# Performance work log

Measured on AMD Instinct MI355X. Metric: run time of the kernel, lower is better.

## Reference

```python
import jax, jax.numpy as jnp
import numpy as np

# dims
B, T, F, R, H = 2048, 50, 64, 6, 64      # batch, time, features, num_rims, hidden per rim
KS, VS = 64, 128                          # input attention key/query size, value size
NC, QC, VC = 4, 32, 16                    # comm heads, comm key/query size, comm value (NC*VC == H)
S = 16                                    # static features
K_ACT = 4                                 # active rims (top-k routing)


def setup_inputs() -> dict:
    key = jax.random.key(0)
    ks = jax.random.split(key, 24)
    f32 = jnp.float32
    rn = lambda k, shape, scale: jax.random.normal(k, shape, f32) * scale
    inp = {}
    inp['x'] = jax.random.normal(ks[0], (B, T, F), f32)
    inp['statics'] = jax.random.normal(ks[1], (B, S), f32)
    inp['mask'] = (jax.random.uniform(ks[2], (B, T, F)) > 0.3).astype(f32)
    inp['delta'] = jax.random.uniform(ks[3], (B, T, F), f32) * 5.0
    inp['x_last_observed'] = jax.random.normal(ks[4], (B, T, F), f32)
    inp['x_mean'] = jax.random.normal(ks[5], (B, F), f32)
    # GRU-D style per-feature input decay params
    inp['w_dg'] = rn(ks[6], (F,), 0.1)
    inp['b_dg'] = jnp.zeros((F,), f32)
    # input attention (shared K/V over the 2-slot [input, null] axis; per-rim group query)
    inp['Wk'] = rn(ks[7], (F, KS), 1.0 / np.sqrt(F))
    inp['Wv'] = rn(ks[8], (F, VS), 1.0 / np.sqrt(F))
    inp['Wq'] = rn(ks[9], (R, H, KS), 1.0 / np.sqrt(H))
    # per-rim (group) GRU cell
    inp['W_ih'] = rn(ks[10], (R, VS, 3 * H), 1.0 / np.sqrt(VS))
    inp['W_hh'] = rn(ks[11], (R, H, 3 * H), 1.0 / np.sqrt(H))
    inp['b_ih'] = jnp.zeros((R, 3 * H), f32)
    inp['b_hh'] = jnp.zeros((R, 3 * H), f32)
    # communication attention (per-rim group projections)
    inp['Wq_c'] = rn(ks[12], (R, H, NC * QC), 1.0 / np.sqrt(H))
    inp['Wk_c'] = rn(ks[13], (R, H, NC * QC), 1.0 / np.sqrt(H))
    inp['Wv_c'] = rn(ks[14], (R, H, NC * VC), 1.0 / np.sqrt(H))
    # MLP head
    inp['W1'] = rn(ks[15], (R * H + S, 10), 1.0 / np.sqrt(R * H + S))
    inp['b1'] = jnp.zeros((10,), f32)
    inp['W2'] = rn(ks[16], (10, 2), 1.0 / np.sqrt(10))
    inp['b2'] = jnp.zeros((2,), f32)
    return inp


def reference(x, statics, mask, delta, x_last_observed, x_mean,
              w_dg, b_dg, Wk, Wv, Wq, W_ih, W_hh, b_ih, b_hh,
              Wq_c, Wk_c, Wv_c, W1, b1, W2, b2):
    Bn = x.shape[0]
    inv_sk = 1.0 / np.sqrt(KS).astype(np.float32)
    inv_sq = 1.0 / np.sqrt(QC).astype(np.float32)

    def step(h, inp_t):
        xt, mt, dt, xlt = inp_t  # each [B,F]
        # GRU-D input decay / imputation
        gamma = jnp.exp(-jax.nn.relu(dt * w_dg + b_dg))
        xh = mt * xt + (1.0 - mt) * (gamma * xlt + (1.0 - gamma) * x_mean)
        # input attention over [real, null] slots
        x_in = jnp.stack([xh, jnp.zeros_like(xh)], axis=1)          # [B,2,F]
        Km = x_in @ Wk                                               # [B,2,KS]
        Vm = x_in @ Wv                                               # [B,2,VS]
        Q = jnp.einsum('brh,rhk->brk', h, Wq)                        # [B,R,KS]
        probs = jax.nn.softmax(jnp.einsum('brk,bnk->brn', Q, Km) * inv_sk, axis=-1)  # [B,R,2]
        inputs = jnp.einsum('brn,bnv->brv', probs, Vm)               # [B,R,VS]
        # top-k active rims = least attention to the null slot
        act_idx = jax.lax.top_k(-probs[:, :, 1], K_ACT)[1]           # [B,K_ACT]
        rim_mask = jnp.sum(jax.nn.one_hot(act_idx, R, dtype=h.dtype), axis=1)  # [B,R]
        # per-rim GRU update (blocked GEMMs)
        gi = jnp.einsum('brv,rvg->brg', inputs, W_ih) + b_ih         # [B,R,3H]
        gh = jnp.einsum('brh,rhg->brg', h, W_hh) + b_hh              # [B,R,3H]
        i_r, i_z, i_n = jnp.split(gi, 3, axis=-1)
        h_r, h_z, h_n = jnp.split(gh, 3, axis=-1)
        r = jax.nn.sigmoid(i_r + h_r)
        z = jax.nn.sigmoid(i_z + h_z)
        n = jnp.tanh(i_n + r * h_n)
        h_new = (1.0 - z) * n + z * h                                # [B,R,H]
        # communication attention among rims
        q = jnp.einsum('brh,rhk->brk', h_new, Wq_c).reshape(Bn, R, NC, QC).transpose(0, 2, 1, 3)
        k = jnp.einsum('brh,rhk->brk', h_new, Wk_c).reshape(Bn, R, NC, QC).transpose(0, 2, 1, 3)
        v = jnp.einsum('brh,rhk->brk', h_new, Wv_c).reshape(Bn, R, NC, VC).transpose(0, 2, 1, 3)
        cprobs = jax.nn.softmax(jnp.einsum('bcrk,bcsk->bcrs', q, k) * inv_sq, axis=-1)  # [B,NC,R,R]
        comm = jnp.einsum('bcrs,bcsv->bcrv', cprobs, v).transpose(0, 2, 1, 3).reshape(Bn, R, NC * VC)
        # only active rims are updated (and receive comm); inactive keep old state
        m = rim_mask[..., None]
        h_out = m * (h_new + comm) + (1.0 - m) * h
        return h_out, None

    h0 = jnp.zeros((Bn, R, H), x.dtype)
    seq = (x.transpose(1, 0, 2), mask.transpose(1, 0, 2),
           delta.transpose(1, 0, 2), x_last_observed.transpose(1, 0, 2))
    hT, _ = jax.lax.scan(step, h0, seq)
    full = jnp.concatenate([hT.reshape(Bn, R * H), statics], axis=1)
    predictions = jax.nn.relu(full @ W1 + b1) @ W2 + b2              # [B,2]
    return predictions
```

## Files before the change

### kernel.cpp

```cpp
#include <hip/hip_runtime.h>
#include <math.h>

#define T_STEPS 50
#define BB 8

__device__ __forceinline__ void fma4(float4& a, const float4 v, const float s) {
  a.x = fmaf(v.x, s, a.x); a.y = fmaf(v.y, s, a.y);
  a.z = fmaf(v.z, s, a.z); a.w = fmaf(v.w, s, a.w);
}
__device__ __forceinline__ float sigmoidf_(float x) { return 1.0f / (1.0f + __expf(-x)); }
__device__ __forceinline__ float tanhf_(float x) {
  float ax = fabsf(x);
  float e = __expf(-2.0f * ax);
  float t = (1.0f - e) / (1.0f + e);
  return copysignf(t, x);
}

__global__ void wcomb_kernel(const float* __restrict__ Wv, const float* __restrict__ Wih,
                             float* __restrict__ Wc) {
  int g = threadIdx.x;
  int f = blockIdx.x & 63;
  int r = blockIdx.x >> 6;
  float acc = 0.f;
#pragma unroll 8
  for (int v = 0; v < 128; ++v)
    acc = fmaf(Wv[f * 128 + v], Wih[(r * 128 + v) * 192 + g], acc);
  Wc[(r * 64 + f) * 192 + g] = acc;
}

__global__ __launch_bounds__(1024, 1) void rims_kernel(
    const float* __restrict__ x, const float* __restrict__ statics,
    const float* __restrict__ maskp, const float* __restrict__ delta,
    const float* __restrict__ xlast, const float* __restrict__ xmean,
    const float* __restrict__ wdgp, const float* __restrict__ bdgp,
    const float* __restrict__ Wk, const float* __restrict__ Wq,
    const float* __restrict__ Whh, const float* __restrict__ bih,
    const float* __restrict__ bhh, const float* __restrict__ Wqc,
    const float* __restrict__ Wkc, const float* __restrict__ Wvc,
    const float* __restrict__ W1, const float* __restrict__ b1,
    const float* __restrict__ W2, const float* __restrict__ b2,
    const float* __restrict__ Wcomb, float* __restrict__ out) {
  __shared__ float xh_T[64][8];
  __shared__ float h_T[6][64][8];
  __shared__ float hn_T[6][64][8];
  __shared__ float K0_R[8][64];
  __shared__ float Q_R[6][8][64];
  __shared__ float qc_R[6][8][128];
  __shared__ float kc_R[6][8][128];
  __shared__ float vc_R[6][8][64];
  __shared__ float p0_l[8][6];
  __shared__ float act_l[8][6];

  const int tid = threadIdx.x;
  const int wave = tid >> 6;
  const int lane = tid & 63;
  const int b0 = blockIdx.x * BB;

  for (int i = tid; i < 6 * 64 * 8; i += 1024) (&h_T[0][0][0])[i] = 0.f;

  const float wdg = wdgp[lane];
  const float bdg = bdgp[lane];
  const float xmv = xmean[(size_t)(b0 + (wave & 7)) * 64 + lane];
  float bir = 0.f, biz = 0.f, bin = 0.f, bhr = 0.f, bhz = 0.f, bhn = 0.f;
  if (wave < 12) {
    const int r = wave >> 1;
    bir = bih[r * 192 + lane]; biz = bih[r * 192 + 64 + lane];
    bin = bih[r * 192 + 128 + lane];
    bhr = bhh[r * 192 + lane]; bhz = bhh[r * 192 + 64 + lane];
    bhn = bhh[r * 192 + 128 + lane];
  }
  __syncthreads();

  for (int t = 0; t < T_STEPS; ++t) {
    if (wave < 8) {
      size_t off = ((size_t)(b0 + wave) * T_STEPS + t) * 64 + lane;
      float xt = x[off], mt = maskp[off], dt = delta[off], xl = xlast[off];
      float gm = __expf(-fmaxf(fmaf(dt, wdg, bdg), 0.f));
      xh_T[lane][wave] = mt * xt + (1.f - mt) * (gm * xl + (1.f - gm) * xmv);
    }
    __syncthreads();
    if (wave < 14) {
      const int p = wave >> 1, q = wave & 1;
      const float* W = (p == 0) ? Wk : (Wq + (p - 1) * 4096);
      const float(*src)[8] = (p == 0) ? xh_T : h_T[p - 1];
      float4 acc = {0, 0, 0, 0};
#pragma unroll 8
      for (int k = 0; k < 64; ++k) {
        float w = W[k * 64 + lane];
        float4 a = *(const float4*)&src[k][q * 4];
        fma4(acc, a, w);
      }
      if (p == 0) {
        K0_R[q * 4 + 0][lane] = acc.x; K0_R[q * 4 + 1][lane] = acc.y;
        K0_R[q * 4 + 2][lane] = acc.z; K0_R[q * 4 + 3][lane] = acc.w;
      } else {
        float(*Qr)[64] = Q_R[p - 1];
        Qr[q * 4 + 0][lane] = acc.x; Qr[q * 4 + 1][lane] = acc.y;
        Qr[q * 4 + 2][lane] = acc.z; Qr[q * 4 + 3][lane] = acc.w;
      }
    }
    __syncthreads();
    if (wave < 8) {
      const int row = wave;
      float k0 = K0_R[row][lane];
      float logit[6];
#pragma unroll
      for (int r = 0; r < 6; ++r) {
        float p = Q_R[r][row][lane] * k0;
#pragma unroll
        for (int d = 1; d < 64; d <<= 1) p += __shfl_xor(p, d, 64);
        logit[r] = p * 0.125f;
      }
      if (lane == 0) {
#pragma unroll
        for (int r = 0; r < 6; ++r) {
          int rank = 0;
#pragma unroll
          for (int r2 = 0; r2 < 6; ++r2)
            rank += (logit[r2] > logit[r]) || (logit[r2] == logit[r] && r2 < r);
          p0_l[row][r] = sigmoidf_(logit[r]);
          act_l[row][r] = (rank < 4) ? 1.f : 0.f;
        }
      }
    }
    __syncthreads();
    if (wave < 12) {
      const int r = wave >> 1, q = wave & 1;
      const float* Wc = Wcomb + r * 12288;
      const float* Wh = Whh + r * 12288;
      float4 ur = {0,0,0,0}, uz = {0,0,0,0}, un = {0,0,0,0};
      float4 gr = {0,0,0,0}, gz = {0,0,0,0}, gn = {0,0,0,0};
#pragma unroll 4
      for (int k = 0; k < 64; ++k) {
        float w0 = Wc[k * 192 + lane], w1 = Wc[k * 192 + 64 + lane],
              w2 = Wc[k * 192 + 128 + lane];
        float v0 = Wh[k * 192 + lane], v1 = Wh[k * 192 + 64 + lane],
              v2 = Wh[k * 192 + 128 + lane];
        float4 xv = *(const float4*)&xh_T[k][q * 4];
        float4 hv = *(const float4*)&h_T[r][k][q * 4];
        fma4(ur, xv, w0); fma4(uz, xv, w1); fma4(un, xv, w2);
        fma4(gr, hv, v0); fma4(gz, hv, v1); fma4(gn, hv, v2);
      }
      float4 hold = *(const float4*)&h_T[r][lane][q * 4];
      auto gru1 = [&](float p0v, float u0, float u1, float u2, float g0, float g1,
                      float g2, float holdv) -> float {
        float rg = sigmoidf_(fmaf(p0v, u0, bir) + g0 + bhr);
        float zg = sigmoidf_(fmaf(p0v, u1, biz) + g1 + bhz);
        float ng = tanhf_(fmaf(p0v, u2, bin) + rg * (g2 + bhn));
        return (1.f - zg) * ng + zg * holdv;
      };
      float4 hn;
      hn.x = gru1(p0_l[q * 4 + 0][r], ur.x, uz.x, un.x, gr.x, gz.x, gn.x, hold.x);
      hn.y = gru1(p0_l[q * 4 + 1][r], ur.y, uz.y, un.y, gr.y, gz.y, gn.y, hold.y);
      hn.z = gru1(p0_l[q * 4 + 2][r], ur.z, uz.z, un.z, gr.z, gz.z, gn.z, hold.z);
      hn.w = gru1(p0_l[q * 4 + 3][r], ur.w, uz.w, un.w, gr.w, gz.w, gn.w, hold.w);
      *(float4*)&hn_T[r][lane][q * 4] = hn;
    }
    __syncthreads();
    for (int u = wave; u < 36; u += 16) {
      if (u < 24) {
        const int v = (u < 12) ? u : (u - 12);
        const int r = v >> 1, q = v & 1;
        const float* W = ((u < 12) ? Wqc : Wkc) + r * 8192;
        float4 a0 = {0,0,0,0}, a1 = {0,0,0,0};
#pragma unroll 4
        for (int k = 0; k < 64; ++k) {
          float w0 = W[k * 128 + lane], w1 = W[k * 128 + 64 + lane];
          float4 a = *(const float4*)&hn_T[r][k][q * 4];
          fma4(a0, a, w0); fma4(a1, a, w1);
        }
        float(*dst)[128] = (u < 12) ? qc_R[r] : kc_R[r];
        dst[q * 4 + 0][lane] = a0.x; dst[q * 4 + 1][lane] = a0.y;
        dst[q * 4 + 2][lane] = a0.z; dst[q * 4 + 3][lane] = a0.w;
        dst[q * 4 + 0][64 + lane] = a1.x; dst[q * 4 + 1][64 + lane] = a1.y;
        dst[q * 4 + 2][64 + lane] = a1.z; dst[q * 4 + 3][64 + lane] = a1.w;
      } else {
        const int v = u - 24;
        const int r = v >> 1, q = v & 1;
        const float* W = Wvc + r * 4096;
        float4 a0 = {0,0,0,0};
#pragma unroll 4
        for (int k = 0; k < 64; ++k) {
          float w = W[k * 64 + lane];
          float4 a = *(const float4*)&hn_T[r][k][q * 4];
          fma4(a0, a, w);
        }
        vc_R[r][q * 4 + 0][lane] = a0.x; vc_R[r][q * 4 + 1][lane] = a0.y;
        vc_R[r][q * 4 + 2][lane] = a0.z; vc_R[r][q * 4 + 3][lane] = a0.w;
      }
    }
    __syncthreads();
    {
      const int row = wave >> 1;
      const int half = wave & 1;
      float kcA[6], kcB[6], vcv[6];
#pragma unroll
      for (int s = 0; s < 6; ++s) {
        kcA[s] = kc_R[s][row][lane];
        kcB[s] = kc_R[s][row][64 + lane];
        vcv[s] = vc_R[s][row][lane];
      }
      const int cOut = lane >> 4;
      const int srcLane = (cOut & 1) << 5;
      const float inv_sq = 0.17677669529663687f;
#pragma unroll
      for (int jr = 0; jr < 3; ++jr) {
        const int rr = half * 3 + jr;
        float qA = qc_R[rr][row][lane], qB = qc_R[rr][row][64 + lane];
        float sL[6], sH[6];
#pragma unroll
        for (int s = 0; s < 6; ++s) {
          float p = qA * kcA[s];
          p += __shfl_xor(p, 1, 64); p += __shfl_xor(p, 2, 64); p += __shfl_xor(p, 4, 64);
          p += __shfl_xor(p, 8, 64); p += __shfl_xor(p, 16, 64);
          sL[s] = p * inv_sq;
          float q = qB * kcB[s];
          q += __shfl_xor(q, 1, 64); q += __shfl_xor(q, 2, 64); q += __shfl_xor(q, 4, 64);
          q += __shfl_xor(q, 8, 64); q += __shfl_xor(q, 16, 64);
          sH[s] = q * inv_sq;
        }
        float mL = sL[0], mH = sH[0];
#pragma unroll
        for (int s = 1; s < 6; ++s) { mL = fmaxf(mL, sL[s]); mH = fmaxf(mH, sH[s]); }
        float sumL = 0.f, sumH = 0.f;
#pragma unroll
        for (int s = 0; s < 6; ++s) {
          sL[s] = __expf(sL[s] - mL); sumL += sL[s];
          sH[s] = __expf(sH[s] - mH); sumH += sH[s];
        }
        float rLn = 1.f / sumL, rHn = 1.f / sumH;
        float comm = 0.f;
#pragma unroll
        for (int s = 0; s < 6; ++s) {
          float tL = __shfl(sL[s] * rLn, srcLane, 64);
          float tH = __shfl(sH[s] * rHn, srcLane, 64);
          float cp = (cOut < 2) ? tL : tH;
          comm = fmaf(cp, vcv[s], comm);
        }
        float mk = act_l[row][rr];
        float hnv = hn_T[rr][lane][row];
        float hov = h_T[rr][lane][row];
        h_T[rr][lane][row] = (mk > 0.5f) ? (hnv + comm) : hov;
      }
    }
    __syncthreads();
  }

  if (wave < 8) {
    const int b = b0 + wave;
    float acc[10];
#pragma unroll
    for (int o = 0; o < 10; ++o) acc[o] = 0.f;
#pragma unroll
    for (int ii = 0; ii < 6; ++ii) {
      float f = h_T[ii][lane][wave];
      const float* w = W1 + (ii * 64 + lane) * 10;
#pragma unroll
      for (int o = 0; o < 10; ++o) acc[o] = fmaf(f, w[o], acc[o]);
    }
    if (lane < 16) {
      float f = statics[(size_t)b * 16 + lane];
      const float* w = W1 + (384 + lane) * 10;
#pragma unroll
      for (int o = 0; o < 10; ++o) acc[o] = fmaf(f, w[o], acc[o]);
    }
#pragma unroll
    for (int o = 0; o < 10; ++o) {
#pragma unroll
      for (int d = 1; d < 64; d <<= 1) acc[o] += __shfl_xor(acc[o], d, 64);
    }
    if (lane == 0) {
      float o0 = b2[0], o1 = b2[1];
#pragma unroll
      for (int o = 0; o < 10; ++o) {
        float a = fmaxf(acc[o] + b1[o], 0.f);
        o0 = fmaf(a, W2[o * 2 + 0], o0);
        o1 = fmaf(a, W2[o * 2 + 1], o1);
      }
      out[(size_t)b * 2 + 0] = o0;
      out[(size_t)b * 2 + 1] = o1;
    }
  }
}

extern "C" void kernel_launch(void* const* d_in, const int* in_sizes, int n_in,
                              void* d_out, int out_size, void* d_ws, size_t ws_size,
                              hipStream_t stream) {
  const float* x       = (const float*)d_in[0];
  const float* statics = (const float*)d_in[1];
  const float* maskp   = (const float*)d_in[2];
  const float* delta   = (const float*)d_in[3];
  const float* xlast   = (const float*)d_in[4];
  const float* xmean   = (const float*)d_in[5];
  const float* wdg     = (const float*)d_in[6];
  const float* bdg     = (const float*)d_in[7];
  const float* Wk      = (const float*)d_in[8];
  const float* Wv      = (const float*)d_in[9];
  const float* Wq      = (const float*)d_in[10];
  const float* Wih     = (const float*)d_in[11];
  const float* Whh     = (const float*)d_in[12];
  const float* bih     = (const float*)d_in[13];
  const float* bhh     = (const float*)d_in[14];
  const float* Wqc     = (const float*)d_in[15];
  const float* Wkc     = (const float*)d_in[16];
  const float* Wvc     = (const float*)d_in[17];
  const float* W1      = (const float*)d_in[18];
  const float* b1      = (const float*)d_in[19];
  const float* W2      = (const float*)d_in[20];
  const float* b2      = (const float*)d_in[21];
  float* Wcomb = (float*)d_ws;

  wcomb_kernel<<<384, 192, 0, stream>>>(Wv, Wih, Wcomb);
  rims_kernel<<<256, 1024, 0, stream>>>(x, statics, maskp, delta, xlast, xmean,
                                        wdg, bdg, Wk, Wq, Whh, bih, bhh,
                                        Wqc, Wkc, Wvc, W1, b1, W2, b2,
                                        Wcomb, (float*)d_out);
}
```

Measured before the change: 1.692 ms.

## Prefetch next-step inputs, split GRU by K halves, pool shared memory

Moves the input imputation for step t+1 into the tail of step t so its global loads overlap the communication phase, which removes one barrier per step. The GRU matmul is split across two waves by halves of the reduction dimension. The split uses partial sums exchanged through shared memory, the p0 scaling is folded into the x operand, and the r/z biases are merged. The projection waves now each cover all 8 batch rows and there are fewer comm projection units (30 instead of 36). Shared buffers are aliased in one pool to reuse space. This adds an extra partial-sum exchange and barrier in the GRU, and some waves carry more work per step.

```diff
diff --git a/kernel.cpp b/kernel.cpp
--- a/kernel.cpp
+++ b/kernel.cpp
@@ -3,10 +3,27 @@
 
 #define T_STEPS 50
 #define BB 8
+
+#define O_XH    0
+#define O_HT    512
+#define O_HNT   3584
+#define O_HNR   6656
+#define O_K0    9728
+#define O_Q     10240
+#define O_QC    13312
+#define O_KC    19456
+#define O_VC    25600
+#define O_P0    28672
+#define O_ACT   28720
+#define O_PART  13312
+#define POOL_F  28768
 
 __device__ __forceinline__ void fma4(float4& a, const float4 v, const float s) {
   a.x = fmaf(v.x, s, a.x); a.y = fmaf(v.y, s, a.y);
   a.z = fmaf(v.z, s, a.z); a.w = fmaf(v.w, s, a.w);
+}
+__device__ __forceinline__ float4 mul4(const float4 a, const float4 b) {
+  return make_float4(a.x * b.x, a.y * b.y, a.z * b.z, a.w * b.w);
 }
 __device__ __forceinline__ float sigmoidf_(float x) { return 1.0f / (1.0f + __expf(-x)); }
 __device__ __forceinline__ float tanhf_(float x) {
@@ -40,73 +57,61 @@
     const float* __restrict__ W1, const float* __restrict__ b1,
     const float* __restrict__ W2, const float* __restrict__ b2,
     const float* __restrict__ Wcomb, float* __restrict__ out) {
-  __shared__ float xh_T[64][8];
-  __shared__ float h_T[6][64][8];
-  __shared__ float hn_T[6][64][8];
-  __shared__ float K0_R[8][64];
-  __shared__ float Q_R[6][8][64];
-  __shared__ float qc_R[6][8][128];
-  __shared__ float kc_R[6][8][128];
-  __shared__ float vc_R[6][8][64];
-  __shared__ float p0_l[8][6];
-  __shared__ float act_l[8][6];
+  __shared__ float pool[POOL_F];
 
   const int tid = threadIdx.x;
   const int wave = tid >> 6;
   const int lane = tid & 63;
   const int b0 = blockIdx.x * BB;
 
-  for (int i = tid; i < 6 * 64 * 8; i += 1024) (&h_T[0][0][0])[i] = 0.f;
+  for (int i = tid; i < 3072; i += 1024) pool[O_HT + i] = 0.f;
 
   const float wdg = wdgp[lane];
   const float bdg = bdgp[lane];
   const float xmv = xmean[(size_t)(b0 + (wave & 7)) * 64 + lane];
-  float bir = 0.f, biz = 0.f, bin = 0.f, bhr = 0.f, bhz = 0.f, bhn = 0.f;
+  float bR = 0.f, bZ = 0.f, bin = 0.f, bhn = 0.f;
   if (wave < 12) {
     const int r = wave >> 1;
-    bir = bih[r * 192 + lane]; biz = bih[r * 192 + 64 + lane];
+    bR = bih[r * 192 + lane] + bhh[r * 192 + lane];
+    bZ = bih[r * 192 + 64 + lane] + bhh[r * 192 + 64 + lane];
     bin = bih[r * 192 + 128 + lane];
-    bhr = bhh[r * 192 + lane]; bhz = bhh[r * 192 + 64 + lane];
     bhn = bhh[r * 192 + 128 + lane];
   }
+  if (wave < 8) {
+    size_t off = ((size_t)(b0 + wave) * T_STEPS + 0) * 64 + lane;
+    float xt = x[off], mt = maskp[off], dt = delta[off], xl = xlast[off];
+    float gm = __expf(-fmaxf(fmaf(dt, wdg, bdg), 0.f));
+    pool[O_XH + lane * 8 + wave] = mt * xt + (1.f - mt) * (gm * xl + (1.f - gm) * xmv);
+  }
   __syncthreads();
 
   for (int t = 0; t < T_STEPS; ++t) {
-    if (wave < 8) {
-      size_t off = ((size_t)(b0 + wave) * T_STEPS + t) * 64 + lane;
-      float xt = x[off], mt = maskp[off], dt = delta[off], xl = xlast[off];
-      float gm = __expf(-fmaxf(fmaf(dt, wdg, bdg), 0.f));
-      xh_T[lane][wave] = mt * xt + (1.f - mt) * (gm * xl + (1.f - gm) * xmv);
-    }
-    __syncthreads();
-    if (wave < 14) {
-      const int p = wave >> 1, q = wave & 1;
+    if (wave < 7) {
+      const int p = wave;
       const float* W = (p == 0) ? Wk : (Wq + (p - 1) * 4096);
-      const float(*src)[8] = (p == 0) ? xh_T : h_T[p - 1];
-      float4 acc = {0, 0, 0, 0};
+      const float* src = (p == 0) ? (pool + O_XH) : (pool + O_HT + (p - 1) * 512);
+      float4 aL = {0, 0, 0, 0}, aH = {0, 0, 0, 0};
 #pragma unroll 8
       for (int k = 0; k < 64; ++k) {
         float w = W[k * 64 + lane];
-        float4 a = *(const float4*)&src[k][q * 4];
-        fma4(acc, a, w);
-      }
-      if (p == 0) {
-        K0_R[q * 4 + 0][lane] = acc.x; K0_R[q * 4 + 1][lane] = acc.y;
-        K0_R[q * 4 + 2][lane] = acc.z; K0_R[q * 4 + 3][lane] = acc.w;
-      } else {
-        float(*Qr)[64] = Q_R[p - 1];
-        Qr[q * 4 + 0][lane] = acc.x; Qr[q * 4 + 1][lane] = acc.y;
-        Qr[q * 4 + 2][lane] = acc.z; Qr[q * 4 + 3][lane] = acc.w;
-      }
+        float4 s0 = *(const float4*)&src[k * 8];
+        float4 s1 = *(const float4*)&src[k * 8 + 4];
+        fma4(aL, s0, w); fma4(aH, s1, w);
+      }
+      float* dst = (p == 0) ? (pool + O_K0) : (pool + O_Q + (p - 1) * 512);
+      dst[0 * 64 + lane] = aL.x; dst[1 * 64 + lane] = aL.y;
+      dst[2 * 64 + lane] = aL.z; dst[3 * 64 + lane] = aL.w;
+      dst[4 * 64 + lane] = aH.x; dst[5 * 64 + lane] = aH.y;
+      dst[6 * 64 + lane] = aH.z; dst[7 * 64 + lane] = aH.w;
     }
     __syncthreads();
     if (wave < 8) {
       const int row = wave;
-      float k0 = K0_R[row][lane];
+      float k0 = pool[O_K0 + row * 64 + lane];
       float logit[6];
 #pragma unroll
       for (int r = 0; r < 6; ++r) {
-        float p = Q_R[r][row][lane] * k0;
+        float p = pool[O_Q + (r * 8 + row) * 64 + lane] * k0;
 #pragma unroll
         for (int d = 1; d < 64; d <<= 1) p += __shfl_xor(p, d, 64);
         logit[r] = p * 0.125f;
@@ -118,87 +123,138 @@
 #pragma unroll
           for (int r2 = 0; r2 < 6; ++r2)
             rank += (logit[r2] > logit[r]) || (logit[r2] == logit[r] && r2 < r);
-          p0_l[row][r] = sigmoidf_(logit[r]);
-          act_l[row][r] = (rank < 4) ? 1.f : 0.f;
+          pool[O_P0 + row * 6 + r] = sigmoidf_(logit[r]);
+          pool[O_ACT + row * 6 + r] = (rank < 4) ? 1.f : 0.f;
         }
       }
     }
     __syncthreads();
+    float4 aR_L, aR_H, aZ_L, aZ_H, aUN_L, aUN_H, aGN_L, aGN_H;
     if (wave < 12) {
-      const int r = wave >> 1, q = wave & 1;
-      const float* Wc = Wcomb + r * 12288;
-      const float* Wh = Whh + r * 12288;
-      float4 ur = {0,0,0,0}, uz = {0,0,0,0}, un = {0,0,0,0};
-      float4 gr = {0,0,0,0}, gz = {0,0,0,0}, gn = {0,0,0,0};
+      const int r = wave >> 1, kh = wave & 1;
+      const float* Wc = Wcomb + r * 12288 + kh * 32 * 192;
+      const float* Wh = Whh + r * 12288 + kh * 32 * 192;
+      const float* xh = pool + O_XH + kh * 32 * 8;
+      const float* hT = pool + O_HT + r * 512 + kh * 32 * 8;
+      float4 p0L = make_float4(pool[O_P0 + 0 * 6 + r], pool[O_P0 + 1 * 6 + r],
+                               pool[O_P0 + 2 * 6 + r], pool[O_P0 + 3 * 6 + r]);
+      float4 p0H = make_float4(pool[O_P0 + 4 * 6 + r], pool[O_P0 + 5 * 6 + r],
+                               pool[O_P0 + 6 * 6 + r], pool[O_P0 + 7 * 6 + r]);
+      aR_L = aR_H = aZ_L = aZ_H = make_float4(0, 0, 0, 0);
+      aUN_L = aUN_H = aGN_L = aGN_H = make_float4(0, 0, 0, 0);
 #pragma unroll 4
-      for (int k = 0; k < 64; ++k) {
+      for (int k = 0; k < 32; ++k) {
         float w0 = Wc[k * 192 + lane], w1 = Wc[k * 192 + 64 + lane],
               w2 = Wc[k * 192 + 128 + lane];
         float v0 = Wh[k * 192 + lane], v1 = Wh[k * 192 + 64 + lane],
               v2 = Wh[k * 192 + 128 + lane];
-        float4 xv = *(const float4*)&xh_T[k][q * 4];
-        float4 hv = *(const float4*)&h_T[r][k][q * 4];
-        fma4(ur, xv, w0); fma4(uz, xv, w1); fma4(un, xv, w2);
-        fma4(gr, hv, v0); fma4(gz, hv, v1); fma4(gn, hv, v2);
-      }
-      float4 hold = *(const float4*)&h_T[r][lane][q * 4];
-      auto gru1 = [&](float p0v, float u0, float u1, float u2, float g0, float g1,
-                      float g2, float holdv) -> float {
-        float rg = sigmoidf_(fmaf(p0v, u0, bir) + g0 + bhr);
-        float zg = sigmoidf_(fmaf(p0v, u1, biz) + g1 + bhz);
-        float ng = tanhf_(fmaf(p0v, u2, bin) + rg * (g2 + bhn));
-        return (1.f - zg) * ng + zg * holdv;
-      };
-      float4 hn;
-      hn.x = gru1(p0_l[q * 4 + 0][r], ur.x, uz.x, un.x, gr.x, gz.x, gn.x, hold.x);
-      hn.y = gru1(p0_l[q * 4 + 1][r], ur.y, uz.y, un.y, gr.y, gz.y, gn.y, hold.y);
-      hn.z = gru1(p0_l[q * 4 + 2][r], ur.z, uz.z, un.z, gr.z, gz.z, gn.z, hold.z);
-      hn.w = gru1(p0_l[q * 4 + 3][r], ur.w, uz.w, un.w, gr.w, gz.w, gn.w, hold.w);
-      *(float4*)&hn_T[r][lane][q * 4] = hn;
-    }
-    __syncthreads();
-    for (int u = wave; u < 36; u += 16) {
-      if (u < 24) {
-        const int v = (u < 12) ? u : (u - 12);
-        const int r = v >> 1, q = v & 1;
-        const float* W = ((u < 12) ? Wqc : Wkc) + r * 8192;
-        float4 a0 = {0,0,0,0}, a1 = {0,0,0,0};
-#pragma unroll 4
-        for (int k = 0; k < 64; ++k) {
-          float w0 = W[k * 128 + lane], w1 = W[k * 128 + 64 + lane];
-          float4 a = *(const float4*)&hn_T[r][k][q * 4];
-          fma4(a0, a, w0); fma4(a1, a, w1);
-        }
-        float(*dst)[128] = (u < 12) ? qc_R[r] : kc_R[r];
-        dst[q * 4 + 0][lane] = a0.x; dst[q * 4 + 1][lane] = a0.y;
-        dst[q * 4 + 2][lane] = a0.z; dst[q * 4 + 3][lane] = a0.w;
-        dst[q * 4 + 0][64 + lane] = a1.x; dst[q * 4 + 1][64 + lane] = a1.y;
-        dst[q * 4 + 2][64 + lane] = a1.z; dst[q * 4 + 3][64 + lane] = a1.w;
+        float4 x0 = *(const float4*)&xh[k * 8];
+        float4 x1 = *(const float4*)&xh[k * 8 + 4];
+        float4 h0 = *(const float4*)&hT[k * 8];
+        float4 h1 = *(const float4*)&hT[k * 8 + 4];
+        float4 xp0 = mul4(x0, p0L);
+        float4 xp1 = mul4(x1, p0H);
+        fma4(aR_L, xp0, w0); fma4(aR_L, h0, v0);
+        fma4(aR_H, xp1, w0); fma4(aR_H, h1, v0);
+        fma4(aZ_L, xp0, w1); fma4(aZ_L, h0, v1);
+        fma4(aZ_H, xp1, w1); fma4(aZ_H, h1, v1);
+        fma4(aUN_L, xp0, w2); fma4(aUN_H, xp1, w2);
+        fma4(aGN_L, h0, v2); fma4(aGN_H, h1, v2);
+      }
+      float* Pp = pool + O_PART + r * 8 * 256;
+      const int orow = (kh == 0) ? 4 : 0;
+      float4 wR = (kh == 0) ? aR_H : aR_L;
+      float4 wZ = (kh == 0) ? aZ_H : aZ_L;
+      float4 wU = (kh == 0) ? aUN_H : aUN_L;
+      float4 wG = (kh == 0) ? aGN_H : aGN_L;
+      Pp[(orow + 0) * 256 + lane] = wR.x; Pp[(orow + 1) * 256 + lane] = wR.y;
+      Pp[(orow + 2) * 256 + lane] = wR.z; Pp[(orow + 3) * 256 + lane] = wR.w;
+      Pp[(orow + 0) * 256 + 64 + lane] = wZ.x; Pp[(orow + 1) * 256 + 64 + lane] = wZ.y;
+      Pp[(orow + 2) * 256 + 64 + lane] = wZ.z; Pp[(orow + 3) * 256 + 64 + lane] = wZ.w;
+      Pp[(orow + 0) * 256 + 128 + lane] = wU.x; Pp[(orow + 1) * 256 + 128 + lane] = wU.y;
+      Pp[(orow + 2) * 256 + 128 + lane] = wU.z; Pp[(orow + 3) * 256 + 128 + lane] = wU.w;
+      Pp[(orow + 0) * 256 + 192 + lane] = wG.x; Pp[(orow + 1) * 256 + 192 + lane] = wG.y;
+      Pp[(orow + 2) * 256 + 192 + lane] = wG.z; Pp[(orow + 3) * 256 + 192 + lane] = wG.w;
+    }
+    __syncthreads();
+    if (wave < 12) {
+      const int r = wave >> 1, kh = wave & 1;
+      const float* Pp = pool + O_PART + r * 8 * 256;
+      const int crow = kh * 4;
+      float oR[4], oZ[4], oU[4], oG[4];
+      {
+        float4 sR = (kh == 0) ? aR_L : aR_H;
+        float4 sZ = (kh == 0) ? aZ_L : aZ_H;
+        float4 sU = (kh == 0) ? aUN_L : aUN_H;
+        float4 sG = (kh == 0) ? aGN_L : aGN_H;
+        oR[0] = sR.x; oR[1] = sR.y; oR[2] = sR.z; oR[3] = sR.w;
+        oZ[0] = sZ.x; oZ[1] = sZ.y; oZ[2] = sZ.z; oZ[3] = sZ.w;
+        oU[0] = sU.x; oU[1] = sU.y; oU[2] = sU.z; oU[3] = sU.w;
+        oG[0] = sG.x; oG[1] = sG.y; oG[2] = sG.z; oG[3] = sG.w;
+      }
+#pragma unroll
+      for (int j = 0; j < 4; ++j) {
+        const int row = crow + j;
+        float cr = oR[j] + Pp[row * 256 + lane];
+        float cz = oZ[j] + Pp[row * 256 + 64 + lane];
+        float un = oU[j] + Pp[row * 256 + 128 + lane];
+        float gn = oG[j] + Pp[row * 256 + 192 + lane];
+        float rg = sigmoidf_(cr + bR);
+        float zg = sigmoidf_(cz + bZ);
+        float ng = tanhf_(un + bin + rg * (gn + bhn));
+        float hold = pool[O_HT + (r * 64 + lane) * 8 + row];
+        float hnv = (1.f - zg) * ng + zg * hold;
+        pool[O_HNT + (r * 64 + lane) * 8 + row] = hnv;
+        pool[O_HNR + (r * 8 + row) * 64 + lane] = hnv;
+      }
+    }
+    __syncthreads();
+    for (int u = wave; u < 30; u += 16) {
+      const float* W; float* dst; int wstride, r;
+      if (u < 12) {
+        r = u >> 1; const int ch = u & 1;
+        W = Wqc + r * 8192 + ch * 64; wstride = 128;
+        dst = pool + O_QC + r * 8 * 128 + ch * 64;
+      } else if (u < 24) {
+        const int v = u - 12; r = v >> 1; const int ch = v & 1;
+        W = Wkc + r * 8192 + ch * 64; wstride = 128;
+        dst = pool + O_KC + r * 8 * 128 + ch * 64;
       } else {
-        const int v = u - 24;
-        const int r = v >> 1, q = v & 1;
-        const float* W = Wvc + r * 4096;
-        float4 a0 = {0,0,0,0};
-#pragma unroll 4
-        for (int k = 0; k < 64; ++k) {
-          float w = W[k * 64 + lane];
-          float4 a = *(const float4*)&hn_T[r][k][q * 4];
-          fma4(a0, a, w);
-        }
-        vc_R[r][q * 4 + 0][lane] = a0.x; vc_R[r][q * 4 + 1][lane] = a0.y;
-        vc_R[r][q * 4 + 2][lane] = a0.z; vc_R[r][q * 4 + 3][lane] = a0.w;
-      }
+        r = u - 24;
+        W = Wvc + r * 4096; wstride = 64;
+        dst = pool + O_VC + r * 8 * 64;
+      }
+      const float* hn = pool + O_HNT + r * 512;
+      float4 aL = {0, 0, 0, 0}, aH = {0, 0, 0, 0};
+#pragma unroll 8
+      for (int k = 0; k < 64; ++k) {
+        float w = W[(size_t)k * wstride + lane];
+        float4 h0 = *(const float4*)&hn[k * 8];
+        float4 h1 = *(const float4*)&hn[k * 8 + 4];
+        fma4(aL, h0, w); fma4(aH, h1, w);
+      }
+      const int ds = (u < 24) ? 128 : 64;
+      dst[0 * ds + lane] = aL.x; dst[1 * ds + lane] = aL.y;
+      dst[2 * ds + lane] = aL.z; dst[3 * ds + lane] = aL.w;
+      dst[4 * ds + lane] = aH.x; dst[5 * ds + lane] = aH.y;
+      dst[6 * ds + lane] = aH.z; dst[7 * ds + lane] = aH.w;
     }
     __syncthreads();
     {
+      float nx = 0.f, nm = 0.f, nd = 0.f, nxl = 0.f;
+      if (wave < 8) {
+        const int tn = (t + 1 < T_STEPS) ? (t + 1) : (T_STEPS - 1);
+        size_t off = ((size_t)(b0 + wave) * T_STEPS + tn) * 64 + lane;
+        nx = x[off]; nm = maskp[off]; nd = delta[off]; nxl = xlast[off];
+      }
       const int row = wave >> 1;
       const int half = wave & 1;
       float kcA[6], kcB[6], vcv[6];
 #pragma unroll
       for (int s = 0; s < 6; ++s) {
-        kcA[s] = kc_R[s][row][lane];
-        kcB[s] = kc_R[s][row][64 + lane];
-        vcv[s] = vc_R[s][row][lane];
+        kcA[s] = pool[O_KC + (s * 8 + row) * 128 + lane];
+        kcB[s] = pool[O_KC + (s * 8 + row) * 128 + 64 + lane];
+        vcv[s] = pool[O_VC + (s * 8 + row) * 64 + lane];
       }
       const int cOut = lane >> 4;
       const int srcLane = (cOut & 1) << 5;
@@ -206,7 +262,8 @@
 #pragma unroll
       for (int jr = 0; jr < 3; ++jr) {
         const int rr = half * 3 + jr;
-        float qA = qc_R[rr][row][lane], qB = qc_R[rr][row][64 + lane];
+        float qA = pool[O_QC + (rr * 8 + row) * 128 + lane];
+        float qB = pool[O_QC + (rr * 8 + row) * 128 + 64 + lane];
         float sL[6], sH[6];
 #pragma unroll
         for (int s = 0; s < 6; ++s) {
@@ -237,10 +294,14 @@
           float cp = (cOut < 2) ? tL : tH;
           comm = fmaf(cp, vcv[s], comm);
         }
-        float mk = act_l[row][rr];
-        float hnv = hn_T[rr][lane][row];
-        float hov = h_T[rr][lane][row];
-        h_T[rr][lane][row] = (mk > 0.5f) ? (hnv + comm) : hov;
+        float mk = pool[O_ACT + row * 6 + rr];
+        float hnv = pool[O_HNR + (rr * 8 + row) * 64 + lane];
+        float hov = pool[O_HT + (rr * 64 + lane) * 8 + row];
+        pool[O_HT + (rr * 64 + lane) * 8 + row] = (mk > 0.5f) ? (hnv + comm) : hov;
+      }
+      if (wave < 8) {
+        float gm = __expf(-fmaxf(fmaf(nd, wdg, bdg), 0.f));
+        pool[O_XH + lane * 8 + wave] = nm * nx + (1.f - nm) * (gm * nxl + (1.f - gm) * xmv);
       }
     }
     __syncthreads();
@@ -253,7 +314,7 @@
     for (int o = 0; o < 10; ++o) acc[o] = 0.f;
 #pragma unroll
     for (int ii = 0; ii < 6; ++ii) {
-      float f = h_T[ii][lane][wave];
+      float f = pool[O_HT + (ii * 64 + lane) * 8 + wave];
       const float* w = W1 + (ii * 64 + lane) * 10;
 #pragma unroll
       for (int o = 0; o < 10; ++o) acc[o] = fmaf(f, w[o], acc[o]);
```

Result: slower. 4.105 ms (+142.7%).
